# Kernel optimization log

Hardware: AMD Instinct MI355X
Metric: run time of the kernel (lower is better)

The kernel has to match this reference:

```python
import jax, jax.numpy as jnp
import numpy as np

R, C = 8192, 8192  # dense shape of the layer's parameter tensor
NE, NN = 4_000_000, 4_000_000


def setup_inputs() -> dict:
    key = jax.random.key(0)
    k1, k2, k3, k4 = jax.random.split(key, 4)
    vals_e = jax.random.normal(k1, (NE,), dtype=jnp.float32)
    vals_n = jax.random.normal(k2, (NN,), dtype=jnp.float32)
    idx_e = jax.random.randint(k3, (2, NE), 0, R, dtype=jnp.int64)
    idx_n = jax.random.randint(k4, (2, NN), 0, R, dtype=jnp.int64)
    return {"vals_e": vals_e, "vals_n": vals_n, "idx_e": idx_e, "idx_n": idx_n}


def reference(vals_e, vals_n, idx_e, idx_n):
    # Sparse COO union with max-abs dedup, expressed as a vectorized
    # scatter-reduce into the dense parameter space (equivalent math:
    # at every index, keep the value with the largest absolute value;
    # untouched positions are 0, matching a sparse representation).
    flat_e = idx_e[0] * C + idx_e[1]  # [NE]
    flat_n = idx_n[0] * C + idx_n[1]  # [NN]
    flat = jnp.concatenate([flat_e, flat_n])            # [NE+NN]
    vals = jnp.concatenate([vals_e, vals_n])            # [NE+NN]

    # pass 1: max |v| per position
    amax = jnp.zeros((R * C,), dtype=vals.dtype).at[flat].max(jnp.abs(vals))
    # pass 2: recover the signed winner (strict-abs winner; ties measure-zero for randn)
    is_winner = jnp.abs(vals) == amax[flat]
    neg_inf = jnp.array(-jnp.inf, dtype=vals.dtype)
    cand = jnp.where(is_winner, vals, neg_inf)
    out = jnp.full((R * C,), neg_inf, dtype=vals.dtype).at[flat].max(cand)
    out = jnp.where(jnp.isneginf(out), jnp.zeros((), dtype=vals.dtype), out)
    return out.reshape(R, C)
```

## Files before the change

kernel.cpp:

```cpp
#include <hip/hip_runtime.h>

#define CDIM     8192
#define NBKT     512
#define BSH      4
#define SLOTS    24
#define SSTR     25
#define PB       8192
#define BINTHR   1024
#define MTHR     1024
#define TWORDS   32768
#define SUBS     4
#define OVFCAP   1024
#define OVFSTR   16
#define MYP4     12

typedef int          vi4 __attribute__((ext_vector_type(4)));
typedef float        vf4 __attribute__((ext_vector_type(4)));
typedef unsigned int vu4 __attribute__((ext_vector_type(4)));

#define NTL(p)    __builtin_nontemporal_load(p)
#define NTS(p, v) __builtin_nontemporal_store((v), (p))

__global__ __launch_bounds__(1024) void k_zinit(unsigned int* __restrict__ g) {
    g[(size_t)blockIdx.x * 1024 + threadIdx.x] = 0u;
}


__global__ __launch_bounds__(BINTHR) void k_bin_v(
    const float* __restrict__ ve, const int* __restrict__ ie, int ne,
    const float* __restrict__ vn, const int* __restrict__ in_, int nn,
    uint2* __restrict__ pairs, unsigned int* __restrict__ ovfcnt,
    uint2* __restrict__ ovf, int nblk)
{
    __shared__ uint2 stage[NBKT * SSTR];
    __shared__ unsigned int hist[NBKT];
    const int tid = threadIdx.x;
    const int total = ne + nn;
    const int start = blockIdx.x * PB;
    const int end = min(total, start + PB);

    for (int b = tid; b < NBKT; b += BINTHR) hist[b] = 0;

    const int iA = start + tid * 4;
    const int iB = iA + BINTHR * 4;
    const bool hasA = iA < end;
    const bool hasB = iB < end;
    vi4 rvA = {0,0,0,0}, cvA = {0,0,0,0}, rvB = {0,0,0,0}, cvB = {0,0,0,0};
    vf4 xvA = {0,0,0,0}, xvB = {0,0,0,0};
    if (hasA) {
        if (iA < ne) {
            rvA = NTL((const vi4*)(ie + iA));
            cvA = NTL((const vi4*)(ie + ne + iA));
            xvA = NTL((const vf4*)(ve + iA));
        } else {
            int j = iA - ne;
            rvA = NTL((const vi4*)(in_ + j));
            cvA = NTL((const vi4*)(in_ + nn + j));
            xvA = NTL((const vf4*)(vn + j));
        }
    }
    if (hasB) {
        if (iB < ne) {
            rvB = NTL((const vi4*)(ie + iB));
            cvB = NTL((const vi4*)(ie + ne + iB));
            xvB = NTL((const vf4*)(ve + iB));
        } else {
            int j = iB - ne;
            rvB = NTL((const vi4*)(in_ + j));
            cvB = NTL((const vi4*)(in_ + nn + j));
            xvB = NTL((const vf4*)(vn + j));
        }
    }
    __syncthreads();

    #pragma unroll
    for (int it = 0; it < 2; ++it) {
        const bool has = it == 0 ? hasA : hasB;
        if (!has) continue;
        const int i0 = it == 0 ? iA : iB;
        const vi4 rv = it == 0 ? rvA : rvB;
        const vi4 cv = it == 0 ? cvA : cvB;
        const vf4 xv = it == 0 ? xvA : xvB;
        const int lim = end - i0;
        #pragma unroll
        for (int q = 0; q < 4; ++q) {
            if (q < lim) {
                int r = rv[q];
                int c = cv[q];
                unsigned int u = __float_as_uint(xv[q]);
                unsigned int key = ((u & 0x7FFFFFFFu) << 1) | (u >> 31);
                if (key) {
                    unsigned int b = (unsigned int)r >> BSH;
                    unsigned int off = (((unsigned int)r & 15u) << 13) | (unsigned int)c;
                    unsigned int rk = atomicAdd(&hist[b], 1u);
                    if (__builtin_expect(rk < SLOTS, 1)) {
                        stage[b * SSTR + rk] = make_uint2(off, key);
                    } else {
                        unsigned int d = atomicAdd(&ovfcnt[(size_t)b * OVFSTR], 1u);
                        if (d < OVFCAP)
                            ovf[(size_t)b * OVFCAP + d] = make_uint2(off, key);
                    }
                }
            }
        }
    }
    __syncthreads();

    const size_t slab = (size_t)nblk * SLOTS;
    for (int c = tid; c < NBKT * SLOTS / 2; c += BINTHR) {
        int l0 = 2 * c;
        int b = l0 / SLOTS;
        int s = l0 % SLOTS;
        unsigned int staged = min(hist[b], (unsigned int)SLOTS);
        uint2 v0 = ((unsigned int)s     < staged) ? stage[b * SSTR + s]     : make_uint2(0u, 0u);
        uint2 v1 = ((unsigned int)s + 1 < staged) ? stage[b * SSTR + s + 1] : make_uint2(0u, 0u);
        vu4 w = {v0.x, v0.y, v1.x, v1.y};
        *(vu4*)(pairs + (size_t)b * slab + (size_t)blockIdx.x * SLOTS + s) = w;
    }
}

__global__ __launch_bounds__(MTHR) void k_merge(
    const uint2* __restrict__ pairs, const unsigned int* __restrict__ ovfcnt,
    const uint2* __restrict__ ovf, unsigned int* __restrict__ out, int nblk)
{
    __shared__ unsigned int lk[TWORDS];
    const int b = blockIdx.x;
    const int tid = threadIdx.x;

    const size_t slab = (size_t)nblk * SLOTS;
    const int n4 = (int)(slab >> 1);
    const vu4* p4 = (const vu4*)(pairs + (size_t)b * slab);

    unsigned int cnt = min(ovfcnt[(size_t)b * OVFSTR], (unsigned int)OVFCAP);
    uint2 ovl = make_uint2(0u, 0u);
    if ((unsigned int)tid < cnt) ovl = ovf[(size_t)b * OVFCAP + tid];

    vu4 myp[MYP4];
    #pragma unroll
    for (int k = 0; k < MYP4; ++k) {
        int i2 = k * MTHR + tid;
        vu4 zz = {0u, 0u, 0u, 0u};
        myp[k] = (i2 < n4) ? p4[i2] : zz;
    }

    vu4 z = {0u, 0u, 0u, 0u};
    for (int sub = 0; sub < SUBS; ++sub) {
        for (int i = tid; i < TWORDS / 4; i += MTHR) ((vu4*)lk)[i] = z;
        __syncthreads();
        #pragma unroll
        for (int k = 0; k < MYP4; ++k) {
            vu4 pr = myp[k];
            if (pr[1] && (pr[0] >> 15) == (unsigned int)sub)
                atomicMax(&lk[pr[0] & 32767u], pr[1]);
            if (pr[3] && (pr[2] >> 15) == (unsigned int)sub)
                atomicMax(&lk[pr[2] & 32767u], pr[3]);
        }
        if (ovl.y && (ovl.x >> 15) == (unsigned int)sub)
            atomicMax(&lk[ovl.x & 32767u], ovl.y);
        __syncthreads();
        size_t ob = (size_t)b * 131072u + (size_t)sub * TWORDS;
        for (int i = tid; i < TWORDS / 4; i += MTHR) {
            vu4 k = ((vu4*)lk)[i];
            k[0] = (k[0] >> 1) | ((k[0] & 1u) << 31);
            k[1] = (k[1] >> 1) | ((k[1] & 1u) << 31);
            k[2] = (k[2] >> 1) | ((k[2] & 1u) << 31);
            k[3] = (k[3] >> 1) | ((k[3] & 1u) << 31);
            NTS((vu4*)(out + ob) + i, k);
        }
        __syncthreads();
    }
}


__global__ void k_zero(uint4* __restrict__ out, int n4) {
    int stride = gridDim.x * blockDim.x;
    uint4 z = {0u, 0u, 0u, 0u};
    for (int i = blockIdx.x * blockDim.x + threadIdx.x; i < n4; i += stride)
        out[i] = z;
}

__global__ void k_scatter(const float* __restrict__ vals_e,
                          const int* __restrict__ idx_e, int ne,
                          const float* __restrict__ vals_n,
                          const int* __restrict__ idx_n, int nn,
                          unsigned int* __restrict__ out) {
    int total = ne + nn;
    int stride = gridDim.x * blockDim.x;
    for (int i = blockIdx.x * blockDim.x + threadIdx.x; i < total; i += stride) {
        const float* v; const int* idx; int j, n;
        if (i < ne) { v = vals_e; idx = idx_e; j = i;      n = ne; }
        else        { v = vals_n; idx = idx_n; j = i - ne; n = nn; }
        float x = v[j];
        unsigned int u = __float_as_uint(x);
        unsigned int key = ((u & 0x7FFFFFFFu) << 1) | (u >> 31);
        if (key) {
            int r = idx[j];
            int c = idx[n + j];
            atomicMax(&out[(size_t)r * CDIM + (size_t)c], key);
        }
    }
}

__global__ void k_decode(uint4* __restrict__ out, int n4) {
    int stride = gridDim.x * blockDim.x;
    for (int i = blockIdx.x * blockDim.x + threadIdx.x; i < n4; i += stride) {
        uint4 k = out[i];
        k.x = (k.x >> 1) | ((k.x & 1u) << 31);
        k.y = (k.y >> 1) | ((k.y & 1u) << 31);
        k.z = (k.z >> 1) | ((k.z & 1u) << 31);
        k.w = (k.w >> 1) | ((k.w & 1u) << 31);
        out[i] = k;
    }
}

extern "C" void kernel_launch(void* const* d_in, const int* in_sizes, int n_in,
                              void* d_out, int out_size, void* d_ws, size_t ws_size,
                              hipStream_t stream) {
    const float* vals_e = (const float*)d_in[0];
    const float* vals_n = (const float*)d_in[1];
    const int*   idx_e  = (const int*)d_in[2];
    const int*   idx_n  = (const int*)d_in[3];
    int ne = in_sizes[0];
    int nn = in_sizes[1];
    int total = ne + nn;
    int nblk = (total + PB - 1) / PB;

    const size_t ovfcnt_bytes = (size_t)NBKT * OVFSTR * sizeof(unsigned int);
    const size_t ovf_bytes    = (size_t)NBKT * OVFCAP * sizeof(uint2);
    const size_t pairs_bytes  = (size_t)NBKT * nblk * SLOTS * sizeof(uint2);
    const size_t ws_need = ovfcnt_bytes + ovf_bytes + pairs_bytes;

    if (ws_size >= ws_need && ((ne | nn) & 3) == 0 && nblk <= 1024) {
        unsigned int* ovfcnt = (unsigned int*)d_ws;
        uint2* ovf   = (uint2*)((char*)d_ws + ovfcnt_bytes);
        uint2* pairs = (uint2*)((char*)d_ws + ovfcnt_bytes + ovf_bytes);

        k_zinit<<<dim3(NBKT * OVFSTR / 1024), dim3(1024), 0, stream>>>(ovfcnt);

        k_bin_v<<<dim3(nblk), dim3(BINTHR), 0, stream>>>(
            vals_e, idx_e, ne, vals_n, idx_n, nn, pairs, ovfcnt, ovf, nblk);
        k_merge<<<dim3(NBKT), dim3(MTHR), 0, stream>>>(
            pairs, ovfcnt, ovf, (unsigned int*)d_out, nblk);
    } else {
        unsigned int* out = (unsigned int*)d_out;
        int n4 = out_size / 4;
        dim3 block(256);
        dim3 grid(2048);
        k_zero<<<grid, block, 0, stream>>>((uint4*)d_out, n4);
        k_scatter<<<grid, block, 0, stream>>>(vals_e, idx_e, ne, vals_n, idx_n, nn, out);
        k_decode<<<grid, block, 0, stream>>>((uint4*)d_out, n4);
    }
}
```

Baseline: 113.3 us.

## Split binning block into two half-passes with smaller per-bucket slot slabs

Each binning block now stages and flushes its 8192 elements in two passes of 4096, each writing a 16-slot slab per bucket, instead of one 24-slot slab for all 8192. Per-pass bucket occupancy is about 8 on average, so 16 slots keeps overflow rare while cutting the padded pair storage written and later read by the merge kernel (32 slots per block instead of 24... actually more total slots but tighter). The merge kernel's per-thread register preload grows to cover the larger slab count. This adds an extra flush, syncs and histogram reset per block, and raises register pressure in the merge.

```diff
diff --git a/kernel.cpp b/kernel.cpp
--- a/kernel.cpp
+++ b/kernel.cpp
@@ -3,8 +3,8 @@
 #define CDIM     8192
 #define NBKT     512
 #define BSH      4
-#define SLOTS    24
-#define SSTR     25
+#define SLOTS    16
+#define SSTR     17
 #define PB       8192
 #define BINTHR   1024
 #define MTHR     1024
@@ -12,7 +12,7 @@
 #define SUBS     4
 #define OVFCAP   1024
 #define OVFSTR   16
-#define MYP4     12
+#define MYP4     16
 
 typedef int          vi4 __attribute__((ext_vector_type(4)));
 typedef float        vf4 __attribute__((ext_vector_type(4)));
@@ -30,7 +30,7 @@
     const float* __restrict__ ve, const int* __restrict__ ie, int ne,
     const float* __restrict__ vn, const int* __restrict__ in_, int nn,
     uint2* __restrict__ pairs, unsigned int* __restrict__ ovfcnt,
-    uint2* __restrict__ ovf, int nblk)
+    uint2* __restrict__ ovf, int nblk2)
 {
     __shared__ uint2 stage[NBKT * SSTR];
     __shared__ unsigned int hist[NBKT];
@@ -74,60 +74,67 @@
     __syncthreads();
 
     #pragma unroll
-    for (int it = 0; it < 2; ++it) {
-        const bool has = it == 0 ? hasA : hasB;
-        if (!has) continue;
-        const int i0 = it == 0 ? iA : iB;
-        const vi4 rv = it == 0 ? rvA : rvB;
-        const vi4 cv = it == 0 ? cvA : cvB;
-        const vf4 xv = it == 0 ? xvA : xvB;
+    for (int pass = 0; pass < 2; ++pass) {
+        const bool has = pass == 0 ? hasA : hasB;
+        const int i0 = pass == 0 ? iA : iB;
+        const vi4 rv = pass == 0 ? rvA : rvB;
+        const vi4 cv = pass == 0 ? cvA : cvB;
+        const vf4 xv = pass == 0 ? xvA : xvB;
         const int lim = end - i0;
-        #pragma unroll
-        for (int q = 0; q < 4; ++q) {
-            if (q < lim) {
-                int r = rv[q];
-                int c = cv[q];
-                unsigned int u = __float_as_uint(xv[q]);
-                unsigned int key = ((u & 0x7FFFFFFFu) << 1) | (u >> 31);
-                if (key) {
-                    unsigned int b = (unsigned int)r >> BSH;
-                    unsigned int off = (((unsigned int)r & 15u) << 13) | (unsigned int)c;
-                    unsigned int rk = atomicAdd(&hist[b], 1u);
-                    if (__builtin_expect(rk < SLOTS, 1)) {
-                        stage[b * SSTR + rk] = make_uint2(off, key);
-                    } else {
-                        unsigned int d = atomicAdd(&ovfcnt[(size_t)b * OVFSTR], 1u);
-                        if (d < OVFCAP)
-                            ovf[(size_t)b * OVFCAP + d] = make_uint2(off, key);
+        if (has) {
+            #pragma unroll
+            for (int q = 0; q < 4; ++q) {
+                if (q < lim) {
+                    int r = rv[q];
+                    int c = cv[q];
+                    unsigned int u = __float_as_uint(xv[q]);
+                    unsigned int key = ((u & 0x7FFFFFFFu) << 1) | (u >> 31);
+                    if (key) {
+                        unsigned int b = (unsigned int)r >> BSH;
+                        unsigned int off = (((unsigned int)r & 15u) << 13) | (unsigned int)c;
+                        unsigned int rk = atomicAdd(&hist[b], 1u);
+                        if (__builtin_expect(rk < SLOTS, 1)) {
+                            stage[b * SSTR + rk] = make_uint2(off, key);
+                        } else {
+                            unsigned int d = atomicAdd(&ovfcnt[(size_t)b * OVFSTR], 1u);
+                            if (d < OVFCAP)
+                                ovf[(size_t)b * OVFCAP + d] = make_uint2(off, key);
+                        }
                     }
                 }
             }
         }
-    }
-    __syncthreads();
-
-    const size_t slab = (size_t)nblk * SLOTS;
-    for (int c = tid; c < NBKT * SLOTS / 2; c += BINTHR) {
-        int l0 = 2 * c;
-        int b = l0 / SLOTS;
-        int s = l0 % SLOTS;
-        unsigned int staged = min(hist[b], (unsigned int)SLOTS);
-        uint2 v0 = ((unsigned int)s     < staged) ? stage[b * SSTR + s]     : make_uint2(0u, 0u);
-        uint2 v1 = ((unsigned int)s + 1 < staged) ? stage[b * SSTR + s + 1] : make_uint2(0u, 0u);
-        vu4 w = {v0.x, v0.y, v1.x, v1.y};
-        *(vu4*)(pairs + (size_t)b * slab + (size_t)blockIdx.x * SLOTS + s) = w;
+        __syncthreads();
+
+        const int vb = 2 * blockIdx.x + pass;
+        const size_t slab = (size_t)nblk2 * SLOTS;
+        for (int c4 = tid; c4 < NBKT * SLOTS / 2; c4 += BINTHR) {
+            int l0 = 2 * c4;
+            int b = l0 >> 4;
+            int s = l0 & 15;
+            unsigned int staged = min(hist[b], (unsigned int)SLOTS);
+            uint2 v0 = ((unsigned int)s     < staged) ? stage[b * SSTR + s]     : make_uint2(0u, 0u);
+            uint2 v1 = ((unsigned int)s + 1 < staged) ? stage[b * SSTR + s + 1] : make_uint2(0u, 0u);
+            vu4 w = {v0.x, v0.y, v1.x, v1.y};
+            *(vu4*)(pairs + (size_t)b * slab + (size_t)vb * SLOTS + s) = w;
+        }
+        __syncthreads();
+        if (pass == 0) {
+            for (int b = tid; b < NBKT; b += BINTHR) hist[b] = 0;
+            __syncthreads();
+        }
     }
 }
 
 __global__ __launch_bounds__(MTHR) void k_merge(
     const uint2* __restrict__ pairs, const unsigned int* __restrict__ ovfcnt,
-    const uint2* __restrict__ ovf, unsigned int* __restrict__ out, int nblk)
+    const uint2* __restrict__ ovf, unsigned int* __restrict__ out, int nblk2)
 {
     __shared__ unsigned int lk[TWORDS];
     const int b = blockIdx.x;
     const int tid = threadIdx.x;
 
-    const size_t slab = (size_t)nblk * SLOTS;
+    const size_t slab = (size_t)nblk2 * SLOTS;
     const int n4 = (int)(slab >> 1);
     const vu4* p4 = (const vu4*)(pairs + (size_t)b * slab);
 
@@ -224,13 +231,14 @@
     int nn = in_sizes[1];
     int total = ne + nn;
     int nblk = (total + PB - 1) / PB;
+    int nblk2 = 2 * nblk;
 
     const size_t ovfcnt_bytes = (size_t)NBKT * OVFSTR * sizeof(unsigned int);
     const size_t ovf_bytes    = (size_t)NBKT * OVFCAP * sizeof(uint2);
-    const size_t pairs_bytes  = (size_t)NBKT * nblk * SLOTS * sizeof(uint2);
+    const size_t pairs_bytes  = (size_t)NBKT * nblk2 * SLOTS * sizeof(uint2);
     const size_t ws_need = ovfcnt_bytes + ovf_bytes + pairs_bytes;
 
-    if (ws_size >= ws_need && ((ne | nn) & 3) == 0 && nblk <= 1024) {
+    if (ws_size >= ws_need && ((ne | nn) & 3) == 0 && nblk2 <= 2048) {
         unsigned int* ovfcnt = (unsigned int*)d_ws;
         uint2* ovf   = (uint2*)((char*)d_ws + ovfcnt_bytes);
         uint2* pairs = (uint2*)((char*)d_ws + ovfcnt_bytes + ovf_bytes);
@@ -238,9 +246,9 @@
         k_zinit<<<dim3(NBKT * OVFSTR / 1024), dim3(1024), 0, stream>>>(ovfcnt);
 
         k_bin_v<<<dim3(nblk), dim3(BINTHR), 0, stream>>>(
-            vals_e, idx_e, ne, vals_n, idx_n, nn, pairs, ovfcnt, ovf, nblk);
+            vals_e, idx_e, ne, vals_n, idx_n, nn, pairs, ovfcnt, ovf, nblk2);
         k_merge<<<dim3(NBKT), dim3(MTHR), 0, stream>>>(
-            pairs, ovfcnt, ovf, (unsigned int*)d_out, nblk);
+            pairs, ovfcnt, ovf, (unsigned int*)d_out, nblk2);
     } else {
         unsigned int* out = (unsigned int*)d_out;
         int n4 = out_size / 4;
```

After: 111.7 us. Within noise of the previous version (-1.4%).
